# Performance work log

Measured on AMD Instinct MI355X. Metric: run time of the kernel, lower is better.

Reference implementation:

```python
import jax, jax.numpy as jnp
import numpy as np

B, C, H, W = 8, 512, 64, 64


def setup_inputs() -> dict:
    key = jax.random.key(0)
    k1, k2, k3, k4 = jax.random.split(key, 4)
    x = jax.random.normal(k1, (B, C, H, W), dtype=jnp.float32)
    spatial_feat = jax.random.normal(k2, (B, C, H, W), dtype=jnp.float32)
    multi_scale_feat = jax.random.normal(k3, (B, C, H, W), dtype=jnp.float32)
    scale = jnp.array(1.0, dtype=jnp.float32)  # nn.Parameter(torch.tensor(1.0))
    conv_w = jax.random.normal(k4, (C, C), dtype=jnp.float32) * 0.02  # 1x1 conv kernel [out,in]
    conv_b = jnp.zeros((C,), dtype=jnp.float32)
    return {"x": x, "spatial_feat": spatial_feat, "multi_scale_feat": multi_scale_feat,
            "scale": scale, "conv_w": conv_w, "conv_b": conv_b}


def reference(x, spatial_feat, multi_scale_feat, scale, conv_w, conv_b):
    Bq, Cq, Hq, Wq = x.shape
    L = Hq * Wq
    query = x.reshape(Bq, Cq, L)                                   # [B,C,L]
    kv = jnp.concatenate([spatial_feat.reshape(Bq, Cq, L),
                          multi_scale_feat.reshape(Bq, Cq, L)], axis=1)  # [B,2C,L]
    # attn = scale * L^-0.5 * (query @ kv^T), channel attention [B,C,2C]
    attn = jnp.einsum('bcl,bkl->bck', query, kv) * (scale * (float(L) ** -0.5))
    attn = jax.nn.softmax(attn, axis=-1)
    fused = jnp.einsum('bck,bkl->bcl', attn, kv).reshape(Bq, Cq, Hq, Wq)  # [B,C,H,W]
    out = jnp.einsum('oc,bchw->bohw', conv_w, fused) + conv_b[None, :, None, None]
    return out
```

## Files before the change

### kernel.cpp

```cpp
#include <hip/hip_runtime.h>

#define Bq   8
#define Cc   512
#define Ll   4096
#define KV2  1024
#define KS   4
#define KSL  (Ll / KS)

typedef _Float16 f16;
typedef __attribute__((ext_vector_type(4))) _Float16 f16x4;
typedef __attribute__((ext_vector_type(8))) _Float16 f16x8;
typedef __attribute__((ext_vector_type(4))) float    f32x4;

typedef const __attribute__((address_space(1))) void* gas_t;
typedef __attribute__((address_space(3))) void*       las_t;

__device__ __forceinline__ void gl16(const f16* g, f16* l) {
    __builtin_amdgcn_global_load_lds((gas_t)g, (las_t)l, 16, 0, 0);
}

__global__ __launch_bounds__(256) void p_cvt(const float* __restrict__ in,
                                             f16* __restrict__ hi, int n4) {
    int i = blockIdx.x * 256 + threadIdx.x;
    if (i >= n4) return;
    float4 v = ((const float4*)in)[i];
    f16x4 hv; hv[0] = (f16)v.x; hv[1] = (f16)v.y; hv[2] = (f16)v.z; hv[3] = (f16)v.w;
    ((f16x4*)hi)[i] = hv;
}

__global__ __launch_bounds__(256) void p_split(const float* __restrict__ in,
                                               f16* __restrict__ hi,
                                               f16* __restrict__ lo, int n4) {
    int i = blockIdx.x * 256 + threadIdx.x;
    if (i >= n4) return;
    float4 v = ((const float4*)in)[i];
    f16 h0 = (f16)v.x, h1 = (f16)v.y, h2 = (f16)v.z, h3 = (f16)v.w;
    f16x4 hv; hv[0] = h0; hv[1] = h1; hv[2] = h2; hv[3] = h3;
    f16x4 lv;
    lv[0] = (f16)(v.x - (float)h0); lv[1] = (f16)(v.y - (float)h1);
    lv[2] = (f16)(v.z - (float)h2); lv[3] = (f16)(v.w - (float)h3);
    ((f16x4*)hi)[i] = hv;
    ((f16x4*)lo)[i] = lv;
}

__global__ __launch_bounds__(256) void p_kv(const float* __restrict__ sp,
                                            const float* __restrict__ ms,
                                            f16* __restrict__ kvhi,
                                            f16* __restrict__ kvt) {
    __shared__ float tile[64][65];
    const int b = blockIdx.z, c0 = blockIdx.y * 64, l0 = blockIdx.x * 64;
    const int t = threadIdx.x;
    const int r = t >> 2, q = t & 3;
    const float* src = (c0 + r < Cc)
        ? sp + ((size_t)b * Cc + c0 + r) * Ll
        : ms + ((size_t)b * Cc + (c0 + r - Cc)) * Ll;
    #pragma unroll
    for (int i = 0; i < 4; ++i) {
        int col = q * 16 + i * 4;
        float4 v = *(const float4*)(src + l0 + col);
        f16x4 hv; hv[0] = (f16)v.x; hv[1] = (f16)v.y; hv[2] = (f16)v.z; hv[3] = (f16)v.w;
        *(f16x4*)&kvhi[((size_t)b * KV2 + c0 + r) * Ll + l0 + col] = hv;
        tile[r][col] = v.x; tile[r][col + 1] = v.y;
        tile[r][col + 2] = v.z; tile[r][col + 3] = v.w;
    }
    __syncthreads();
    const int ln = t >> 3, q8 = t & 7;
    #pragma unroll
    for (int p = 0; p < 2; ++p) {
        const int l = ln + 32 * p;
        f16x8 o;
        #pragma unroll
        for (int j = 0; j < 8; ++j) o[j] = (f16)tile[q8 * 8 + j][l];
        *(f16x8*)&kvt[((size_t)b * Ll + l0 + l) * KV2 + c0 + q8 * 8] = o;
    }
}

template<int KD, int NBN, int EPI, bool LO, int KSV>
__global__ __launch_bounds__(256, 3) void gemm_mfma(
    const f16* __restrict__ Ah, const f16* __restrict__ Al, size_t sAb, int lda,
    const f16* __restrict__ Bh, size_t sBb, int ldb,
    const float* __restrict__ scale_ptr, const float* __restrict__ bias,
    float* __restrict__ Cf, f16* __restrict__ Chi,
    size_t sCb, size_t sliceC, int ldc)
{
    __shared__ __align__(16) f16 sA[128 * 64];
    __shared__ __align__(16) f16 sB[128 * 64];
    __shared__ __align__(16) f16 sL[LO ? 128 * 64 : 8];

    int wg = blockIdx.x;
    const int chunk = (int)gridDim.x >> 3;
    wg = (wg & 7) * chunk + (wg >> 3);
    const int m0 = (wg & 3) * 128; wg >>= 2;
    const int n0 = (wg % NBN) * 128; wg /= NBN;
    const int b  = wg / KSV, s = wg % KSV;

    const int t = threadIdx.x;
    const int w = t >> 6, lane = t & 63;
    const int quad = lane >> 4, lr = lane & 15;
    const int wm = (w & 1) * 64, wn = (w >> 1) * 64;
    const int sr = lane >> 3, sc = lane & 7;
    const int swb = (sc ^ sr) << 3;
    const int x7 = lr & 7;

    const f16* gA = Ah + (size_t)b * sAb + (size_t)s * KD
                  + (size_t)(m0 + w * 8 + sr) * lda + swb;
    const f16* gB = Bh + (size_t)b * sBb + (size_t)s * KD
                  + (size_t)(n0 + w * 8 + sr) * ldb + swb;
    const f16* gL = LO ? (Al + (size_t)(m0 + w * 8 + sr) * lda + swb) : nullptr;

    f32x4 acc[4][4];
    #pragma unroll
    for (int i = 0; i < 4; ++i)
        #pragma unroll
        for (int j = 0; j < 4; ++j) {
            acc[i][j][0] = 0.f; acc[i][j][1] = 0.f;
            acc[i][j][2] = 0.f; acc[i][j][3] = 0.f;
        }

    for (int k0 = 0; k0 < KD; k0 += 64) {
        #pragma unroll
        for (int i = 0; i < 4; ++i) {
            gl16(gA + k0 + (size_t)(i * 32) * lda, &sA[(i * 32 + w * 8) * 64]);
            gl16(gB + k0 + (size_t)(i * 32) * ldb, &sB[(i * 32 + w * 8) * 64]);
            if constexpr (LO)
                gl16(gL + k0 + (size_t)(i * 32) * lda, &sL[(i * 32 + w * 8) * 64]);
        }
        asm volatile("s_waitcnt vmcnt(0)" ::: "memory");
        __syncthreads();
        #pragma unroll
        for (int ks = 0; ks < 2; ++ks) {
            f16x8 af[4], bf[4];
            #pragma unroll
            for (int i = 0; i < 4; ++i)
                af[i] = *(const f16x8*)&sA[(wm + i * 16 + lr) * 64
                         + ((((ks << 2) | quad) ^ x7) << 3)];
            #pragma unroll
            for (int j = 0; j < 4; ++j)
                bf[j] = *(const f16x8*)&sB[(wn + j * 16 + lr) * 64
                         + ((((ks << 2) | quad) ^ x7) << 3)];
            #pragma unroll
            for (int i = 0; i < 4; ++i)
                #pragma unroll
                for (int j = 0; j < 4; ++j)
                    acc[i][j] = __builtin_amdgcn_mfma_f32_16x16x32_f16(
                                    af[i], bf[j], acc[i][j], 0, 0, 0);
            if constexpr (LO) {
                f16x8 lf[4];
                #pragma unroll
                for (int i = 0; i < 4; ++i)
                    lf[i] = *(const f16x8*)&sL[(wm + i * 16 + lr) * 64
                             + ((((ks << 2) | quad) ^ x7) << 3)];
                #pragma unroll
                for (int i = 0; i < 4; ++i)
                    #pragma unroll
                    for (int j = 0; j < 4; ++j)
                        acc[i][j] = __builtin_amdgcn_mfma_f32_16x16x32_f16(
                                        lf[i], bf[j], acc[i][j], 0, 0, 0);
            }
        }
        __syncthreads();
    }

    if constexpr (EPI == 0) {
        const float alpha = scale_ptr[0] * 0.015625f;
        f16* Cs = Chi + (size_t)s * sliceC + (size_t)b * sCb;
        #pragma unroll
        for (int i = 0; i < 4; ++i)
            #pragma unroll
            for (int j = 0; j < 4; ++j) {
                const int n = n0 + wn + j * 16 + lr;
                #pragma unroll
                for (int r = 0; r < 4; ++r) {
                    const int m = m0 + wm + i * 16 + quad * 4 + r;
                    Cs[(size_t)m * ldc + n] = (f16)(alpha * acc[i][j][r]);
                }
            }
    } else if constexpr (EPI == 1) {
        f16* Cs = Chi + (size_t)b * sCb;
        #pragma unroll
        for (int i = 0; i < 4; ++i)
            #pragma unroll
            for (int j = 0; j < 4; ++j) {
                const int n = n0 + wn + j * 16 + lr;
                #pragma unroll
                for (int r = 0; r < 4; ++r) {
                    const int m = m0 + wm + i * 16 + quad * 4 + r;
                    Cs[(size_t)m * ldc + n] = (f16)acc[i][j][r];
                }
            }
    } else {
        float* Co = Cf + (size_t)b * sCb;
        #pragma unroll
        for (int i = 0; i < 4; ++i)
            #pragma unroll
            for (int j = 0; j < 4; ++j) {
                const int n = n0 + wn + j * 16 + lr;
                #pragma unroll
                for (int r = 0; r < 4; ++r) {
                    const int m = m0 + wm + i * 16 + quad * 4 + r;
                    Co[(size_t)m * ldc + n] = acc[i][j][r] + bias[m];
                }
            }
    }
}

__global__ __launch_bounds__(256) void k2_softmax_t(const f16* __restrict__ attnP,
                                                    f16* __restrict__ attnT) {
    __shared__ float rmax[16], rinv[16];
    __shared__ __align__(16) f16 tile[16][68];
    const int b = blockIdx.y, c0 = blockIdx.x * 16;
    const int t = threadIdx.x, w = t >> 6, lane = t & 63;
    const size_t sS = (size_t)Bq * Cc * KV2;

    for (int rr = 0; rr < 4; ++rr) {
        const int r = w * 4 + rr;
        const f16* base = attnP + ((size_t)b * Cc + c0 + r) * KV2;
        float v[16];
        #pragma unroll
        for (int i = 0; i < 2; ++i) {
            f16x8 u = *(const f16x8*)(base + (lane + 64 * i) * 8);
            #pragma unroll
            for (int j = 0; j < 8; ++j) v[i * 8 + j] = (float)u[j];
        }
        #pragma unroll
        for (int s = 1; s < KS; ++s) {
            const f16* bs = base + (size_t)s * sS;
            #pragma unroll
            for (int i = 0; i < 2; ++i) {
                f16x8 u = *(const f16x8*)(bs + (lane + 64 * i) * 8);
                #pragma unroll
                for (int j = 0; j < 8; ++j) v[i * 8 + j] += (float)u[j];
            }
        }
        float m = -3.4e38f;
        #pragma unroll
        for (int i = 0; i < 16; ++i) m = fmaxf(m, v[i]);
        #pragma unroll
        for (int off = 32; off; off >>= 1) m = fmaxf(m, __shfl_xor(m, off));
        float s = 0.f;
        #pragma unroll
        for (int i = 0; i < 16; ++i) s += __expf(v[i] - m);
        #pragma unroll
        for (int off = 32; off; off >>= 1) s += __shfl_xor(s, off);
        if (lane == 0) { rmax[r] = m; rinv[r] = 1.0f / s; }
    }
    __syncthreads();

    const int r2 = t >> 4, cn = (t & 15) * 4;
    const int n4 = t >> 2, q = t & 3;
    for (int nt = 0; nt < 16; ++nt) {
        const f16* base = attnP + ((size_t)b * Cc + c0 + r2) * KV2 + nt * 64 + cn;
        float vx[4];
        {
            f16x4 u = *(const f16x4*)base;
            #pragma unroll
            for (int j = 0; j < 4; ++j) vx[j] = (float)u[j];
        }
        #pragma unroll
        for (int s = 1; s < KS; ++s) {
            f16x4 u = *(const f16x4*)(base + (size_t)s * sS);
            #pragma unroll
            for (int j = 0; j < 4; ++j) vx[j] += (float)u[j];
        }
        const float m = rmax[r2], iv = rinv[r2];
        f16x4 hv;
        hv[0] = (f16)(__expf(vx[0] - m) * iv); hv[1] = (f16)(__expf(vx[1] - m) * iv);
        hv[2] = (f16)(__expf(vx[2] - m) * iv); hv[3] = (f16)(__expf(vx[3] - m) * iv);
        *(f16x4*)&tile[r2][cn] = hv;
        __syncthreads();
        f16x4 o;
        o[0] = tile[q * 4 + 0][n4]; o[1] = tile[q * 4 + 1][n4];
        o[2] = tile[q * 4 + 2][n4]; o[3] = tile[q * 4 + 3][n4];
        *(f16x4*)&attnT[((size_t)b * KV2 + nt * 64 + n4) * Cc + c0 + q * 4] = o;
        __syncthreads();
    }
}

#define BM 64
#define BN 64
#define BK 32
#define PAD 4

__device__ __forceinline__ const float* kv_row(const float* __restrict__ sp,
                                               const float* __restrict__ ms,
                                               int b, int k) {
    return (k < Cc) ? (sp + ((size_t)b * Cc + k) * Ll)
                    : (ms + ((size_t)b * Cc + (k - Cc)) * Ll);
}

__global__ __launch_bounds__(256) void k1_logits(const float* __restrict__ x,
                                                 const float* __restrict__ sp,
                                                 const float* __restrict__ ms,
                                                 const float* __restrict__ scale,
                                                 float* __restrict__ attn) {
    __shared__ __align__(16) float As[BK][BM + PAD];
    __shared__ __align__(16) float Bs[BK][BN + PAD];
    const int b = blockIdx.z, m0 = blockIdx.y * BM, n0 = blockIdx.x * BN;
    const int t = threadIdx.x, tx = t & 15, ty = t >> 4, q = t & 7, r = t >> 3;
    const float alpha = scale[0] * (1.0f / 64.0f);
    const float* Abase = x + (size_t)b * Cc * Ll;
    float acc[4][4] = {};
    for (int k0 = 0; k0 < Ll; k0 += BK) {
        #pragma unroll
        for (int hh = 0; hh < 2; ++hh) {
            const int rw = r + 32 * hh;
            float4 v = *(const float4*)(Abase + (size_t)(m0 + rw) * Ll + k0 + 4 * q);
            As[4*q+0][rw] = v.x; As[4*q+1][rw] = v.y; As[4*q+2][rw] = v.z; As[4*q+3][rw] = v.w;
        }
        #pragma unroll
        for (int hh = 0; hh < 2; ++hh) {
            const int rw = r + 32 * hh;
            const float* Brow = kv_row(sp, ms, b, n0 + rw);
            float4 v = *(const float4*)(Brow + k0 + 4 * q);
            Bs[4*q+0][rw] = v.x; Bs[4*q+1][rw] = v.y; Bs[4*q+2][rw] = v.z; Bs[4*q+3][rw] = v.w;
        }
        __syncthreads();
        #pragma unroll
        for (int k = 0; k < BK; ++k) {
            float a[4], bb[4];
            *(float4*)a  = *(const float4*)&As[k][4 * ty];
            *(float4*)bb = *(const float4*)&Bs[k][4 * tx];
            #pragma unroll
            for (int i = 0; i < 4; ++i)
                #pragma unroll
                for (int j = 0; j < 4; ++j) acc[i][j] += a[i] * bb[j];
        }
        __syncthreads();
    }
    #pragma unroll
    for (int i = 0; i < 4; ++i) {
        const int m = m0 + 4 * ty + i;
        float4 o;
        o.x = alpha * acc[i][0]; o.y = alpha * acc[i][1];
        o.z = alpha * acc[i][2]; o.w = alpha * acc[i][3];
        *(float4*)(attn + ((size_t)b * Cc + m) * KV2 + n0 + 4 * tx) = o;
    }
}

__global__ __launch_bounds__(256) void k2_softmax(float* __restrict__ attn) {
    float* p = attn + (size_t)blockIdx.x * KV2;
    const int t = threadIdx.x, lane = t & 63, wv = t >> 6;
    float4 v = ((const float4*)p)[t];
    float m = fmaxf(fmaxf(v.x, v.y), fmaxf(v.z, v.w));
    #pragma unroll
    for (int off = 32; off; off >>= 1) m = fmaxf(m, __shfl_down(m, off));
    __shared__ float redm[4];
    if (lane == 0) redm[wv] = m;
    __syncthreads();
    m = fmaxf(fmaxf(redm[0], redm[1]), fmaxf(redm[2], redm[3]));
    v.x = __expf(v.x - m); v.y = __expf(v.y - m);
    v.z = __expf(v.z - m); v.w = __expf(v.w - m);
    float s = v.x + v.y + v.z + v.w;
    #pragma unroll
    for (int off = 32; off; off >>= 1) s += __shfl_down(s, off);
    __shared__ float reds[4];
    if (lane == 0) reds[wv] = s;
    __syncthreads();
    s = reds[0] + reds[1] + reds[2] + reds[3];
    const float inv = 1.0f / s;
    v.x *= inv; v.y *= inv; v.z *= inv; v.w *= inv;
    ((float4*)p)[t] = v;
}

__global__ __launch_bounds__(256) void k3_wattn(const float* __restrict__ W,
                                                const float* __restrict__ attn,
                                                float* __restrict__ attn2) {
    __shared__ __align__(16) float As[BK][BM + PAD];
    __shared__ __align__(16) float Bs[BK][BN];
    const int b = blockIdx.z, m0 = blockIdx.y * BM, n0 = blockIdx.x * BN;
    const int t = threadIdx.x, tx = t & 15, ty = t >> 4;
    const int q = t & 7, r = t >> 3, c4 = t & 15, kr = t >> 4;
    const float* Bbase = attn + (size_t)b * Cc * KV2;
    float acc[4][4] = {};
    for (int k0 = 0; k0 < Cc; k0 += BK) {
        #pragma unroll
        for (int hh = 0; hh < 2; ++hh) {
            const int rw = r + 32 * hh;
            float4 v = *(const float4*)(W + (size_t)(m0 + rw) * Cc + k0 + 4 * q);
            As[4*q+0][rw] = v.x; As[4*q+1][rw] = v.y; As[4*q+2][rw] = v.z; As[4*q+3][rw] = v.w;
        }
        #pragma unroll
        for (int hh = 0; hh < 2; ++hh) {
            const int k = kr + 16 * hh;
            float4 v = *(const float4*)(Bbase + (size_t)(k0 + k) * KV2 + n0 + 4 * c4);
            *(float4*)&Bs[k][4 * c4] = v;
        }
        __syncthreads();
        #pragma unroll
        for (int k = 0; k < BK; ++k) {
            float a[4], bb[4];
            *(float4*)a  = *(const float4*)&As[k][4 * ty];
            *(float4*)bb = *(const float4*)&Bs[k][4 * tx];
            #pragma unroll
            for (int i = 0; i < 4; ++i)
                #pragma unroll
                for (int j = 0; j < 4; ++j) acc[i][j] += a[i] * bb[j];
        }
        __syncthreads();
    }
    #pragma unroll
    for (int i = 0; i < 4; ++i) {
        const int m = m0 + 4 * ty + i;
        float4 o;
        o.x = acc[i][0]; o.y = acc[i][1]; o.z = acc[i][2]; o.w = acc[i][3];
        *(float4*)(attn2 + ((size_t)b * Cc + m) * KV2 + n0 + 4 * tx) = o;
    }
}

__global__ __launch_bounds__(256) void k4_out(const float* __restrict__ attn2,
                                              const float* __restrict__ sp,
                                              const float* __restrict__ ms,
                                              const float* __restrict__ bias,
                                              float* __restrict__ out) {
    __shared__ __align__(16) float As[BK][BM + PAD];
    __shared__ __align__(16) float Bs[BK][BN];
    const int b = blockIdx.z, m0 = blockIdx.y * BM, n0 = blockIdx.x * BN;
    const int t = threadIdx.x, tx = t & 15, ty = t >> 4;
    const int q = t & 7, r = t >> 3, c4 = t & 15, kr = t >> 4;
    const float* Abase = attn2 + (size_t)b * Cc * KV2;
    float acc[4][4] = {};
    for (int k0 = 0; k0 < KV2; k0 += BK) {
        #pragma unroll
        for (int hh = 0; hh < 2; ++hh) {
            const int rw = r + 32 * hh;
            float4 v = *(const float4*)(Abase + (size_t)(m0 + rw) * KV2 + k0 + 4 * q);
            As[4*q+0][rw] = v.x; As[4*q+1][rw] = v.y; As[4*q+2][rw] = v.z; As[4*q+3][rw] = v.w;
        }
        #pragma unroll
        for (int hh = 0; hh < 2; ++hh) {
            const int k = kr + 16 * hh;
            const float* Brow = kv_row(sp, ms, b, k0 + k);
            float4 v = *(const float4*)(Brow + n0 + 4 * c4);
            *(float4*)&Bs[k][4 * c4] = v;
        }
        __syncthreads();
        #pragma unroll
        for (int k = 0; k < BK; ++k) {
            float a[4], bb[4];
            *(float4*)a  = *(const float4*)&As[k][4 * ty];
            *(float4*)bb = *(const float4*)&Bs[k][4 * tx];
            #pragma unroll
            for (int i = 0; i < 4; ++i)
                #pragma unroll
                for (int j = 0; j < 4; ++j) acc[i][j] += a[i] * bb[j];
        }
        __syncthreads();
    }
    #pragma unroll
    for (int i = 0; i < 4; ++i) {
        const int m = m0 + 4 * ty + i;
        const float bm = bias[m];
        float4 o;
        o.x = acc[i][0] + bm; o.y = acc[i][1] + bm;
        o.z = acc[i][2] + bm; o.w = acc[i][3] + bm;
        *(float4*)(out + ((size_t)b * Cc + m) * Ll + n0 + 4 * tx) = o;
    }
}

extern "C" void kernel_launch(void* const* d_in, const int* in_sizes, int n_in,
                              void* d_out, int out_size, void* d_ws, size_t ws_size,
                              hipStream_t stream) {
    const float* x     = (const float*)d_in[0];
    const float* sp    = (const float*)d_in[1];
    const float* ms    = (const float*)d_in[2];
    const float* scale = (const float*)d_in[3];
    const float* W     = (const float*)d_in[4];
    const float* bias  = (const float*)d_in[5];
    float* out = (float*)d_out;

    const size_t NEED = 219152384;
    if (ws_size >= NEED) {
        char* ws = (char*)d_ws;
        f16* attnP = (f16*)ws;
        f16* Xhi   = (f16*)(ws + 33554432);
        f16* KVhi  = (f16*)(ws + 67108864);
        f16* KVT   = (f16*)(ws + 134217728);
        f16* Whi   = (f16*)(ws + 201326592);
        f16* Wlo   = (f16*)(ws + 201850880);
        f16* attnT = (f16*)(ws + 202375168);
        f16* A2hi  = (f16*)(ws + 210763776);

        dim3 blk(256);
        p_cvt  <<<dim3(16384),                 blk, 0, stream>>>(x, Xhi, Bq * Cc * Ll / 4);
        p_kv   <<<dim3(Ll / 64, KV2 / 64, Bq), blk, 0, stream>>>(sp, ms, KVhi, KVT);
        p_split<<<dim3(256),                   blk, 0, stream>>>(W, Whi, Wlo, Cc * Cc / 4);

        gemm_mfma<KSL, KV2 / 128, 0, false, KS>
            <<<dim3(4 * (KV2 / 128) * Bq * KS), blk, 0, stream>>>(
            Xhi, nullptr, (size_t)Cc * Ll, Ll,
            KVhi, (size_t)KV2 * Ll, Ll,
            scale, nullptr, nullptr, attnP,
            (size_t)Cc * KV2, (size_t)Bq * Cc * KV2, KV2);

        k2_softmax_t<<<dim3(Cc / 16, Bq), blk, 0, stream>>>(attnP, attnT);

        gemm_mfma<Cc, KV2 / 128, 1, true, 1>
            <<<dim3(4 * (KV2 / 128) * Bq), blk, 0, stream>>>(
            Whi, Wlo, (size_t)0, Cc,
            attnT, (size_t)KV2 * Cc, Cc,
            nullptr, nullptr, nullptr, A2hi,
            (size_t)Cc * KV2, (size_t)0, KV2);

        gemm_mfma<KV2, Ll / 128, 2, false, 1>
            <<<dim3(4 * (Ll / 128) * Bq), blk, 0, stream>>>(
            A2hi, nullptr, (size_t)Cc * KV2, KV2,
            KVT, (size_t)Ll * KV2, KV2,
            nullptr, bias, out, nullptr,
            (size_t)Cc * Ll, (size_t)0, Ll);
    } else {
        float* attn  = (float*)d_ws;
        float* attn2 = attn + (size_t)Bq * Cc * KV2;
        dim3 blk(256);
        k1_logits <<<dim3(KV2 / BN, Cc / BM, Bq), blk, 0, stream>>>(x, sp, ms, scale, attn);
        k2_softmax<<<dim3(Bq * Cc),               blk, 0, stream>>>(attn);
        k3_wattn  <<<dim3(KV2 / BN, Cc / BM, Bq), blk, 0, stream>>>(W, attn, attn2);
        k4_out    <<<dim3(Ll / BN, Cc / BM, Bq), blk, 0, stream>>>(attn2, sp, ms, bias, out);
    }
}
```

Measured before the change: 381.4 us.

## Add 256x256-tile 8-wave GEMM with LDS ring pipeline for logits and output GEMMs

Adds a new gemm256 kernel that uses 512 threads and 256x256 output tiles. It stages A and B halves through an 8-slot LDS ring with global_load_lds, prefetching two tiles ahead and interleaving MFMA phases with barriers and setprio. The logits GEMM and the final output GEMM now use it instead of the 128x128 gemm_mfma, aiming for more data reuse per block and overlap of loads with compute. The cost is higher register and LDS pressure (128KB of LDS per block), fewer blocks in the grid, and a tricky hand-written wait/barrier schedule that could race.

```diff
diff --git a/kernel.cpp b/kernel.cpp
--- a/kernel.cpp
+++ b/kernel.cpp
@@ -75,6 +75,185 @@
     }
 }
 
+template<int KD, int NBN, int EPI, int KSV>
+__global__ __launch_bounds__(512, 2) void gemm256(
+    const f16* __restrict__ Ah, size_t sAb, int lda,
+    const f16* __restrict__ Bh, size_t sBb, int ldb,
+    const float* __restrict__ scale_ptr, const float* __restrict__ bias,
+    float* __restrict__ Cf, f16* __restrict__ Chi,
+    size_t sCb, size_t sliceC, int ldc)
+{
+    constexpr int NT = KD / 64;
+    __shared__ __align__(16) f16 ring[8][128 * 64];
+
+    int wg = blockIdx.x;
+    const int chunk = (int)gridDim.x >> 3;
+    wg = (wg & 7) * chunk + (wg >> 3);
+    const int m0 = (wg & 1) * 256; wg >>= 1;
+    const int n0 = (wg % NBN) * 256; wg /= NBN;
+    const int b = wg / KSV, s = wg % KSV;
+
+    const int t = threadIdx.x;
+    const int w = t >> 6, lane = t & 63;
+    const int quad = lane >> 4, lr = lane & 15;
+    const int wm = (w >> 2) * 128, wn = (w & 3) * 64;
+    const int tA = 2 + (w >> 2);
+    const int tB = (w & 3) >> 1;
+    const int brow = (w & 1) * 64;
+    const int srow = lane >> 3, sslot = (lane & 7) ^ srow;
+    const int x7 = lr & 7;
+
+    const f16* gA = Ah + (size_t)b * sAb + (size_t)s * KD
+                  + (size_t)(m0 + w * 8 + srow) * lda + sslot * 8;
+    const f16* gB = Bh + (size_t)b * sBb + (size_t)s * KD
+                  + (size_t)(n0 + w * 8 + srow) * ldb + sslot * 8;
+    f16* const ld0 = &ring[0][0] + (w * 8) * 64;
+
+    auto stA = [&](int tile, int half) {
+        if (tile >= NT) return;
+        f16* d = ld0 + ((tile * 4 + 2 + half) & 7) * (128 * 64);
+        const f16* g = gA + (size_t)(half * 128) * lda + tile * 64;
+        gl16(g, d);
+        gl16(g + (size_t)64 * lda, d + 64 * 64);
+    };
+    auto stB = [&](int tile, int half) {
+        if (tile >= NT) return;
+        f16* d = ld0 + ((tile * 4 + half) & 7) * (128 * 64);
+        const f16* g = gB + (size_t)(half * 128) * ldb + tile * 64;
+        gl16(g, d);
+        gl16(g + (size_t)64 * ldb, d + 64 * 64);
+    };
+
+    f32x4 acc[8][4];
+    #pragma unroll
+    for (int i = 0; i < 8; ++i)
+        #pragma unroll
+        for (int j = 0; j < 4; ++j) {
+            acc[i][j][0] = 0.f; acc[i][j][1] = 0.f;
+            acc[i][j][2] = 0.f; acc[i][j][3] = 0.f;
+        }
+
+    stB(0, 0); stB(0, 1); stA(0, 0); stA(0, 1);
+    stB(1, 0); stB(1, 1); stA(1, 0);
+    asm volatile("s_waitcnt vmcnt(6)" ::: "memory");
+    __builtin_amdgcn_s_barrier();
+
+    f16x8 a[4][2], bf[4][2];
+
+    #pragma unroll 2
+    for (int T = 0; T < NT; ++T) {
+        const f16* sAp = &ring[(T * 4 + tA) & 7][0];
+        const f16* sBp = &ring[(T * 4 + tB) & 7][0];
+
+        #pragma unroll
+        for (int ii = 0; ii < 4; ++ii)
+            #pragma unroll
+            for (int ks = 0; ks < 2; ++ks)
+                a[ii][ks] = *(const f16x8*)&sAp[(ii * 16 + lr) * 64
+                             + ((((ks << 2) | quad) ^ x7) << 3)];
+        #pragma unroll
+        for (int j = 0; j < 4; ++j)
+            #pragma unroll
+            for (int ks = 0; ks < 2; ++ks)
+                bf[j][ks] = *(const f16x8*)&sBp[(brow + j * 16 + lr) * 64
+                             + ((((ks << 2) | quad) ^ x7) << 3)];
+        stA(T + 1, 1);
+        asm volatile("s_waitcnt lgkmcnt(0)" ::: "memory");
+        __builtin_amdgcn_s_barrier();
+        __builtin_amdgcn_s_setprio(1);
+        #pragma unroll
+        for (int ii = 0; ii < 4; ++ii)
+            #pragma unroll
+            for (int j = 0; j < 2; ++j)
+                #pragma unroll
+                for (int ks = 0; ks < 2; ++ks)
+                    acc[ii][j] = __builtin_amdgcn_mfma_f32_16x16x32_f16(
+                                     a[ii][ks], bf[j][ks], acc[ii][j], 0, 0, 0);
+        __builtin_amdgcn_s_setprio(0);
+        __builtin_amdgcn_s_barrier();
+
+        stB(T + 2, 0);
+        __builtin_amdgcn_s_barrier();
+        __builtin_amdgcn_s_setprio(1);
+        #pragma unroll
+        for (int ii = 0; ii < 4; ++ii)
+            #pragma unroll
+            for (int j = 0; j < 2; ++j)
+                #pragma unroll
+                for (int ks = 0; ks < 2; ++ks)
+                    acc[ii][2 + j] = __builtin_amdgcn_mfma_f32_16x16x32_f16(
+                                     a[ii][ks], bf[2 + j][ks], acc[ii][2 + j], 0, 0, 0);
+        __builtin_amdgcn_s_setprio(0);
+        __builtin_amdgcn_s_barrier();
+
+        #pragma unroll
+        for (int ii = 0; ii < 4; ++ii)
+            #pragma unroll
+            for (int ks = 0; ks < 2; ++ks)
+                a[ii][ks] = *(const f16x8*)&sAp[((ii + 4) * 16 + lr) * 64
+                             + ((((ks << 2) | quad) ^ x7) << 3)];
+        stB(T + 2, 1);
+        asm volatile("s_waitcnt lgkmcnt(0)" ::: "memory");
+        __builtin_amdgcn_s_barrier();
+        __builtin_amdgcn_s_setprio(1);
+        #pragma unroll
+        for (int ii = 0; ii < 4; ++ii)
+            #pragma unroll
+            for (int j = 0; j < 2; ++j)
+                #pragma unroll
+                for (int ks = 0; ks < 2; ++ks)
+                    acc[4 + ii][j] = __builtin_amdgcn_mfma_f32_16x16x32_f16(
+                                     a[ii][ks], bf[j][ks], acc[4 + ii][j], 0, 0, 0);
+        __builtin_amdgcn_s_setprio(0);
+        __builtin_amdgcn_s_barrier();
+
+        stA(T + 2, 0);
+        if (T + 2 < NT) { asm volatile("s_waitcnt vmcnt(6)" ::: "memory"); }
+        else            { asm volatile("s_waitcnt vmcnt(0)" ::: "memory"); }
+        __builtin_amdgcn_s_barrier();
+        __builtin_amdgcn_s_setprio(1);
+        #pragma unroll
+        for (int ii = 0; ii < 4; ++ii)
+            #pragma unroll
+            for (int j = 0; j < 2; ++j)
+                #pragma unroll
+                for (int ks = 0; ks < 2; ++ks)
+                    acc[4 + ii][2 + j] = __builtin_amdgcn_mfma_f32_16x16x32_f16(
+                                     a[ii][ks], bf[2 + j][ks], acc[4 + ii][2 + j], 0, 0, 0);
+        __builtin_amdgcn_s_setprio(0);
+        __builtin_amdgcn_s_barrier();
+    }
+
+    if constexpr (EPI == 0) {
+        const float alpha = scale_ptr[0] * 0.015625f;
+        f16* Cs = Chi + (size_t)s * sliceC + (size_t)b * sCb;
+        #pragma unroll
+        for (int i = 0; i < 8; ++i)
+            #pragma unroll
+            for (int j = 0; j < 4; ++j) {
+                const int n = n0 + wn + j * 16 + lr;
+                #pragma unroll
+                for (int r = 0; r < 4; ++r) {
+                    const int m = m0 + wm + i * 16 + quad * 4 + r;
+                    Cs[(size_t)m * ldc + n] = (f16)(alpha * acc[i][j][r]);
+                }
+            }
+    } else {
+        float* Co = Cf + (size_t)b * sCb;
+        #pragma unroll
+        for (int i = 0; i < 8; ++i)
+            #pragma unroll
+            for (int j = 0; j < 4; ++j) {
+                const int n = n0 + wn + j * 16 + lr;
+                #pragma unroll
+                for (int r = 0; r < 4; ++r) {
+                    const int m = m0 + wm + i * 16 + quad * 4 + r;
+                    Co[(size_t)m * ldc + n] = acc[i][j][r] + bias[m];
+                }
+            }
+    }
+}
+
 template<int KD, int NBN, int EPI, bool LO, int KSV>
 __global__ __launch_bounds__(256, 3) void gemm_mfma(
     const f16* __restrict__ Ah, const f16* __restrict__ Al, size_t sAb, int lda,
@@ -129,21 +308,21 @@
         __syncthreads();
         #pragma unroll
         for (int ks = 0; ks < 2; ++ks) {
-            f16x8 af[4], bf[4];
+            f16x8 af[4], bfr[4];
             #pragma unroll
             for (int i = 0; i < 4; ++i)
                 af[i] = *(const f16x8*)&sA[(wm + i * 16 + lr) * 64
                          + ((((ks << 2) | quad) ^ x7) << 3)];
             #pragma unroll
             for (int j = 0; j < 4; ++j)
-                bf[j] = *(const f16x8*)&sB[(wn + j * 16 + lr) * 64
+                bfr[j] = *(const f16x8*)&sB[(wn + j * 16 + lr) * 64
                          + ((((ks << 2) | quad) ^ x7) << 3)];
             #pragma unroll
             for (int i = 0; i < 4; ++i)
                 #pragma unroll
                 for (int j = 0; j < 4; ++j)
                     acc[i][j] = __builtin_amdgcn_mfma_f32_16x16x32_f16(
-                                    af[i], bf[j], acc[i][j], 0, 0, 0);
+                                    af[i], bfr[j], acc[i][j], 0, 0, 0);
             if constexpr (LO) {
                 f16x8 lf[4];
                 #pragma unroll
@@ -155,7 +334,7 @@
                     #pragma unroll
                     for (int j = 0; j < 4; ++j)
                         acc[i][j] = __builtin_amdgcn_mfma_f32_16x16x32_f16(
-                                        lf[i], bf[j], acc[i][j], 0, 0, 0);
+                                        lf[i], bfr[j], acc[i][j], 0, 0, 0);
             }
         }
         __syncthreads();
@@ -485,9 +664,9 @@
         p_kv   <<<dim3(Ll / 64, KV2 / 64, Bq), blk, 0, stream>>>(sp, ms, KVhi, KVT);
         p_split<<<dim3(256),                   blk, 0, stream>>>(W, Whi, Wlo, Cc * Cc / 4);
 
-        gemm_mfma<KSL, KV2 / 128, 0, false, KS>
-            <<<dim3(4 * (KV2 / 128) * Bq * KS), blk, 0, stream>>>(
-            Xhi, nullptr, (size_t)Cc * Ll, Ll,
+        gemm256<KSL, KV2 / 256, 0, KS>
+            <<<dim3(2 * (KV2 / 256) * Bq * KS), dim3(512), 0, stream>>>(
+            Xhi, (size_t)Cc * Ll, Ll,
             KVhi, (size_t)KV2 * Ll, Ll,
             scale, nullptr, nullptr, attnP,
             (size_t)Cc * KV2, (size_t)Bq * Cc * KV2, KV2);
@@ -501,9 +680,9 @@
             nullptr, nullptr, nullptr, A2hi,
             (size_t)Cc * KV2, (size_t)0, KV2);
 
-        gemm_mfma<KV2, Ll / 128, 2, false, 1>
-            <<<dim3(4 * (Ll / 128) * Bq), blk, 0, stream>>>(
-            A2hi, nullptr, (size_t)Cc * KV2, KV2,
+        gemm256<KV2, Ll / 256, 2, 1>
+            <<<dim3(2 * (Ll / 256) * Bq), dim3(512), 0, stream>>>(
+            A2hi, (size_t)Cc * KV2, KV2,
             KVT, (size_t)Ll * KV2, KV2,
             nullptr, bias, out, nullptr,
             (size_t)Cc * Ll, (size_t)0, Ll);
```

After: 344.6 us. 1.11x faster.
